# Optimization experiments

Measured on AMD Instinct MI355X. Metric: run time of the kernel, lower is better.

## Reference

```python
import jax, jax.numpy as jnp
import numpy as np
import math

TAU = math.log(2.0)   # C=2
LAM = 0.25
BATCH_SIZE = 12


def _lambertw(y, iters=20):
    """Principal-branch Lambert W for y >= -1/e via Halley iteration (on-device,
    replacing the scipy CPU roundtrip)."""
    # initial guess: series expansion near the branch point, log1p elsewhere
    w = jnp.where(
        y < 1.0,
        -1.0 + jnp.sqrt(jnp.maximum(2.0 * (jnp.e * y + 1.0), 0.0)),
        jnp.log1p(y),
    )

    def body(w, _):
        ew = jnp.exp(w)
        f = w * ew - y
        denom = ew * (w + 1.0) - (w + 2.0) * f / (2.0 * (w + 1.0) + 1e-12)
        w = jnp.where(jnp.abs(f) > 0.0, w - f / denom, w)
        return w, None

    w, _ = jax.lax.scan(body, w, None, length=iters)
    return w


def setup_inputs() -> dict:
    key = jax.random.key(0)
    n = 2097152  # rows per label group
    logits = jax.random.normal(key, (3 * n, 3), dtype=jnp.float32)
    return {"discriminator_out": logits, "n0": n, "n1": n, "n2": n}


def reference(discriminator_out, n0, n1, n2):
    # labels: n0 zeros, n1 ones, n2 twos (static sizes)
    labels = jnp.concatenate([
        jnp.zeros((n0,), jnp.int32),
        jnp.ones((n1,), jnp.int32),
        jnp.full((n2,), 2, jnp.int32),
    ])
    # per-row cross entropy (single log_softmax shared by both CE uses in the torch code)
    logp = jax.nn.log_softmax(discriminator_out, axis=-1)
    l_i = -jnp.take_along_axis(logp, labels[:, None], axis=1)[:, 0]  # [N]

    # sigma uses detached losses
    l_det = jax.lax.stop_gradient(l_i)
    y = 0.5 * jnp.maximum(-2.0 / jnp.e, (l_det - TAU) / LAM)  # y >= -1/e
    w = _lambertw(y)
    sigma = jnp.exp(-w)  # log(sigma) = -w

    loss = ((l_i - TAU) * sigma + LAM * jnp.square(w)).sum() / BATCH_SIZE
    return loss
```

## Files before the change

### kernel.cpp

```cpp
#include <hip/hip_runtime.h>
#include <math.h>

#define TBL_N     1024
#define TBL_MAXU  1023.999f
#define KIDX      44.36141955583649f
#define LOG2E     1.44269504088896340736f
#define INV_BATCH (1.0f / 12.0f)

struct TblData { float v[TBL_N + 1]; };

constexpr double k_ln2 = 0.69314718055994530942;
constexpr double k_e   = 2.71828182845904523536;

constexpr double cexp(double x) {
    double t = x * 1.44269504088896340736;
    int n = (int)(t + (t >= 0 ? 0.5 : -0.5));
    double r = x - (double)n * k_ln2;
    double s = 1.0, term = 1.0;
    for (int i = 1; i <= 13; ++i) { term *= r / i; s += term; }
    double p = 1.0;
    if (n >= 0) for (int i = 0; i <  n; ++i) p *= 2.0;
    else        for (int i = 0; i < -n; ++i) p *= 0.5;
    return s * p;
}
constexpr double csqrt_(double x) {
    double r = x > 1.0 ? x : 1.0;
    for (int i = 0; i < 24; ++i) r = 0.5 * (r + x / r);
    return r;
}
constexpr double clog_(double x) {
    int n = 0; double m = x;
    while (m >= 2.0) { m *= 0.5; ++n; }
    while (m <  1.0) { m *= 2.0; --n; }
    double z = (m - 1.0) / (m + 1.0), z2 = z * z, s = 0.0, t = z;
    for (int i = 0; i < 17; ++i) { s += t / (2 * i + 1); t *= z2; }
    return 2.0 * s + (double)n * k_ln2;
}
constexpr TblData make_table() {
    TblData T{};
    for (int i = 0; i <= TBL_N; ++i) {
        double l   = (double)i * (16.0 / TBL_N);
        double tau = k_ln2;
        double l0  = tau - 1.0 / (2.0 * k_e);
        double F;
        if (l < l0) {
            F = k_e * (l - tau) + 0.25;
        } else {
            double y = 2.0 * (l - tau);
            double ylim = -1.0 / k_e;
            if (y < ylim) y = ylim;
            double w = (y < 3.0) ? (csqrt_(2.0 * (k_e * y + 1.0)) - 1.0)
                                 : clog_(y);
            for (int it = 0; it < 4; ++it) {
                double ew  = cexp(w);
                double f   = w * ew - y;
                double wp1 = w + 1.0;
                double den = ew * wp1 - (w + 2.0) * f / (2.0 * wp1 + 1e-300);
                if (f != 0.0) w -= f / den;
            }
            F = 0.25 * ((1.0 + w) * (1.0 + w) - 1.0);
        }
        T.v[i] = (float)F;
    }
    return T;
}
__device__ __constant__ TblData c_tbl = make_table();

__shared__ float s_tbl[TBL_N + 1];

__device__ __forceinline__ float tbl_eval(float u) {
    u = fminf(u, TBL_MAXU);
    int   i = (int)u;
    float f = u - (float)i;
    float t0 = s_tbl[i];
    float t1 = s_tbl[i + 1];
    return fmaf(f, t1 - t0, t0);
}

template<int L>
__device__ __forceinline__ float row_fixed(float a, float b, float c) {
    float xl = (L == 0) ? a : ((L == 1) ? b : c);
    float o1 = (L == 0) ? b : a;
    float o2 = (L == 2) ? b : c;
    float e1 = exp2f((o1 - xl) * LOG2E);
    float e2 = exp2f((o2 - xl) * LOG2E);
    float u  = __log2f(1.0f + e1 + e2) * KIDX;
    return tbl_eval(u);
}

__device__ __forceinline__ float row_gen(float a, float b, float c, int lab) {
    float xl = (lab == 0) ? a : ((lab == 1) ? b : c);
    float o1 = (lab == 0) ? b : a;
    float o2 = (lab == 2) ? b : c;
    float e1 = exp2f((o1 - xl) * LOG2E);
    float e2 = exp2f((o2 - xl) * LOG2E);
    float u  = __log2f(1.0f + e1 + e2) * KIDX;
    return tbl_eval(u);
}

template<int L>
__device__ __forceinline__ float quad_sum(float4 f0, float4 f1, float4 f2) {
    return row_fixed<L>(f0.x, f0.y, f0.z) + row_fixed<L>(f0.w, f1.x, f1.y)
         + row_fixed<L>(f1.z, f1.w, f2.x) + row_fixed<L>(f2.y, f2.z, f2.w);
}

__device__ __forceinline__ float block_reduce(float acc) {
#pragma unroll
    for (int off = 32; off > 0; off >>= 1)
        acc += __shfl_down(acc, off, 64);
    __shared__ float sacc[4];
    int lane = threadIdx.x & 63;
    int wv   = threadIdx.x >> 6;
    if (lane == 0) sacc[wv] = acc;
    __syncthreads();
    float s = 0.0f;
    if (threadIdx.x == 0)
        s = sacc[0] + sacc[1] + sacc[2] + sacc[3];
    return s;
}

__global__ __launch_bounds__(256) void superloss_partial(
        const float* __restrict__ x,
        const int* __restrict__ pn0,
        const int* __restrict__ pn1,
        float* __restrict__ partial,
        int nrows) {
    for (int i = threadIdx.x; i <= TBL_N; i += 256)
        s_tbl[i] = c_tbl.v[i];
    __syncthreads();

    const int n0  = *pn0;
    const int n01 = n0 + *pn1;

    const int gid    = blockIdx.x * 256 + threadIdx.x;
    const int stride = gridDim.x * 256;
    const int nq     = nrows >> 2;

    float acc = 0.0f;

    if (((n0 | n01) & 3) == 0) {
        const int nq0 = n0 >> 2, nq1 = n01 >> 2;
        int q0 = gid, q1 = nq0 + gid, q2 = nq1 + gid;
        for (;;) {
            bool h0 = q0 < nq0, h1 = q1 < nq1, h2 = q2 < nq;
            if (!(h0 || h1 || h2)) break;
            float4 A0, A1, A2, B0, B1, B2, C0, C1, C2;
            if (h0) { const float4* p = (const float4*)x + 3 * (size_t)q0; A0 = p[0]; A1 = p[1]; A2 = p[2]; }
            if (h1) { const float4* p = (const float4*)x + 3 * (size_t)q1; B0 = p[0]; B1 = p[1]; B2 = p[2]; }
            if (h2) { const float4* p = (const float4*)x + 3 * (size_t)q2; C0 = p[0]; C1 = p[1]; C2 = p[2]; }
            if (h0) acc += quad_sum<0>(A0, A1, A2);
            if (h1) acc += quad_sum<1>(B0, B1, B2);
            if (h2) acc += quad_sum<2>(C0, C1, C2);
            q0 += stride; q1 += stride; q2 += stride;
        }
        for (int r = (nq << 2) + gid; r < nrows; r += stride) {
            int lab = (r >= n0) + (r >= n01);
            acc += row_gen(x[3 * (size_t)r], x[3 * (size_t)r + 1],
                           x[3 * (size_t)r + 2], lab);
        }
    } else {
        for (int r = gid; r < nrows; r += stride) {
            int lab = (r >= n0) + (r >= n01);
            acc += row_gen(x[3 * (size_t)r], x[3 * (size_t)r + 1],
                           x[3 * (size_t)r + 2], lab);
        }
    }

    float s = block_reduce(acc);
    if (threadIdx.x == 0)
        partial[blockIdx.x] = s;
}

__global__ __launch_bounds__(256) void superloss_final(
        const float* __restrict__ partial,
        int np,
        float* __restrict__ out) {
    float acc = 0.0f;
    for (int i = threadIdx.x; i < np; i += 256)
        acc += partial[i];
    float s = block_reduce(acc);
    if (threadIdx.x == 0)
        out[0] = s * INV_BATCH;
}

extern "C" void kernel_launch(void* const* d_in, const int* in_sizes, int n_in,
                              void* d_out, int out_size, void* d_ws, size_t ws_size,
                              hipStream_t stream) {
    const float* x   = (const float*)d_in[0];
    const int*   pn0 = (const int*)d_in[1];
    const int*   pn1 = (const int*)d_in[2];

    const int nrows = in_sizes[0] / 3;

    int nblk = 2048;
    size_t need = (size_t)nblk * sizeof(float);
    if (ws_size < need) {
        nblk = (int)(ws_size / sizeof(float));
        if (nblk < 1) nblk = 1;
    }

    float* partial = (float*)d_ws;
    superloss_partial<<<nblk, 256, 0, stream>>>(x, pn0, pn1, partial, nrows);
    superloss_final<<<1, 256, 0, stream>>>(partial, nblk, (float*)d_out);
}
```

Measured before the change: 109.1 us.

## Index loss table by float exponent bits, drop log and interpolation

Replaces the log2-plus-linear-interpolation lookup with a 2048-entry table indexed directly by the top mantissa and exponent bits of the softmax denominator, so each row skips the log and one of its two shared-memory reads. The 1/12 scale is folded into the table. The three interleaved label regions are now walked in separate loops instead of one combined loop. Without interpolation the piecewise-constant lookup adds approximation error, and the region loops lose the interleaving of loads across regions.

Measured after the change: 105.4 us. 3.4% less time.

```diff
diff --git a/kernel.cpp b/kernel.cpp
--- a/kernel.cpp
+++ b/kernel.cpp
@@ -1,13 +1,12 @@
 #include <hip/hip_runtime.h>
 #include <math.h>
 
-#define TBL_N     1024
-#define TBL_MAXU  1023.999f
-#define KIDX      44.36141955583649f
+#define NTB       2048
 #define LOG2E     1.44269504088896340736f
-#define INV_BATCH (1.0f / 12.0f)
-
-struct TblData { float v[TBL_N + 1]; };
+#define IDX_BIAS  0x3F80u
+#define INV_BATCH (1.0 / 12.0)
+
+struct alignas(16) TblData { float v[NTB]; };
 
 constexpr double k_ln2 = 0.69314718055994530942;
 constexpr double k_e   = 2.71828182845904523536;
@@ -25,7 +24,7 @@
 }
 constexpr double csqrt_(double x) {
     double r = x > 1.0 ? x : 1.0;
-    for (int i = 0; i < 24; ++i) r = 0.5 * (r + x / r);
+    for (int i = 0; i < 12; ++i) r = 0.5 * (r + x / r);
     return r;
 }
 constexpr double clog_(double x) {
@@ -38,70 +37,80 @@
 }
 constexpr TblData make_table() {
     TblData T{};
-    for (int i = 0; i <= TBL_N; ++i) {
-        double l   = (double)i * (16.0 / TBL_N);
-        double tau = k_ln2;
-        double l0  = tau - 1.0 / (2.0 * k_e);
+    const double tau = k_ln2;
+    const double l0  = tau - 1.0 / (2.0 * k_e);
+    double w_prev = 0.0;
+    for (int i = 0; i < NTB; ++i) {
+        int e = i >> 7, m = i & 127;
+        double s = 1.0 + ((double)m + 0.5) / 128.0;
+        for (int k = 0; k < e; ++k) s *= 2.0;
+        double l = clog_(s);
         double F;
         if (l < l0) {
             F = k_e * (l - tau) + 0.25;
         } else {
             double y = 2.0 * (l - tau);
-            double ylim = -1.0 / k_e;
-            if (y < ylim) y = ylim;
-            double w = (y < 3.0) ? (csqrt_(2.0 * (k_e * y + 1.0)) - 1.0)
-                                 : clog_(y);
-            for (int it = 0; it < 4; ++it) {
-                double ew  = cexp(w);
-                double f   = w * ew - y;
-                double wp1 = w + 1.0;
-                double den = ew * wp1 - (w + 2.0) * f / (2.0 * wp1 + 1e-300);
-                if (f != 0.0) w -= f / den;
+            double w;
+            double dy = y + 1.0 / k_e;
+            if (dy < 0.15) {
+                double p = csqrt_(2.0 * k_e * dy);
+                w = -1.0 + p - p * p / 3.0 + (11.0 / 72.0) * p * p * p;
+            } else {
+                w = w_prev;
             }
-            F = 0.25 * ((1.0 + w) * (1.0 + w) - 1.0);
+            for (int it = 0; it < 2; ++it) {
+                double ew = cexp(w);
+                w -= (w * ew - y) / (ew * (w + 1.0));
+            }
+            w_prev = w;
+            F = 0.5 * w + 0.25 * w * w;
         }
-        T.v[i] = (float)F;
+        T.v[i] = (float)(F * INV_BATCH);
     }
     return T;
 }
 __device__ __constant__ TblData c_tbl = make_table();
 
-__shared__ float s_tbl[TBL_N + 1];
-
-__device__ __forceinline__ float tbl_eval(float u) {
-    u = fminf(u, TBL_MAXU);
-    int   i = (int)u;
-    float f = u - (float)i;
-    float t0 = s_tbl[i];
-    float t1 = s_tbl[i + 1];
-    return fmaf(f, t1 - t0, t0);
-}
-
 template<int L>
-__device__ __forceinline__ float row_fixed(float a, float b, float c) {
+__device__ __forceinline__ float row_fixed(const float* __restrict__ tbl,
+                                           float a, float b, float c) {
     float xl = (L == 0) ? a : ((L == 1) ? b : c);
     float o1 = (L == 0) ? b : a;
     float o2 = (L == 2) ? b : c;
-    float e1 = exp2f((o1 - xl) * LOG2E);
-    float e2 = exp2f((o2 - xl) * LOG2E);
-    float u  = __log2f(1.0f + e1 + e2) * KIDX;
-    return tbl_eval(u);
-}
-
-__device__ __forceinline__ float row_gen(float a, float b, float c, int lab) {
+    float s  = 1.0f + exp2f((o1 - xl) * LOG2E) + exp2f((o2 - xl) * LOG2E);
+    unsigned i = (__float_as_uint(s) >> 16) - IDX_BIAS;
+    i = min(i, (unsigned)(NTB - 1));
+    return tbl[i];
+}
+
+__device__ __forceinline__ float row_gen(const float* __restrict__ tbl,
+                                         float a, float b, float c, int lab) {
     float xl = (lab == 0) ? a : ((lab == 1) ? b : c);
     float o1 = (lab == 0) ? b : a;
     float o2 = (lab == 2) ? b : c;
-    float e1 = exp2f((o1 - xl) * LOG2E);
-    float e2 = exp2f((o2 - xl) * LOG2E);
-    float u  = __log2f(1.0f + e1 + e2) * KIDX;
-    return tbl_eval(u);
+    float s  = 1.0f + exp2f((o1 - xl) * LOG2E) + exp2f((o2 - xl) * LOG2E);
+    unsigned i = (__float_as_uint(s) >> 16) - IDX_BIAS;
+    i = min(i, (unsigned)(NTB - 1));
+    return tbl[i];
 }
 
 template<int L>
-__device__ __forceinline__ float quad_sum(float4 f0, float4 f1, float4 f2) {
-    return row_fixed<L>(f0.x, f0.y, f0.z) + row_fixed<L>(f0.w, f1.x, f1.y)
-         + row_fixed<L>(f1.z, f1.w, f2.x) + row_fixed<L>(f2.y, f2.z, f2.w);
+__device__ __forceinline__ float region_sum(const float* __restrict__ x,
+                                            const float* __restrict__ tbl,
+                                            int qlo, int qhi,
+                                            int gid, int stride) {
+    float acc = 0.0f;
+    for (int q = qlo + gid; q < qhi; q += stride) {
+        const float4* p = (const float4*)x + 3 * (size_t)q;
+        float4 f0 = p[0];
+        float4 f1 = p[1];
+        float4 f2 = p[2];
+        acc += row_fixed<L>(tbl, f0.x, f0.y, f0.z);
+        acc += row_fixed<L>(tbl, f0.w, f1.x, f1.y);
+        acc += row_fixed<L>(tbl, f1.z, f1.w, f2.x);
+        acc += row_fixed<L>(tbl, f2.y, f2.z, f2.w);
+    }
+    return acc;
 }
 
 __device__ __forceinline__ float block_reduce(float acc) {
@@ -125,43 +134,38 @@
         const int* __restrict__ pn1,
         float* __restrict__ partial,
         int nrows) {
-    for (int i = threadIdx.x; i <= TBL_N; i += 256)
-        s_tbl[i] = c_tbl.v[i];
+    __shared__ float s_tbl[NTB];
+    {
+        const float4* ct = (const float4*)c_tbl.v;
+        float4* st = (float4*)s_tbl;
+        st[threadIdx.x]       = ct[threadIdx.x];
+        st[threadIdx.x + 256] = ct[threadIdx.x + 256];
+    }
     __syncthreads();
 
     const int n0  = *pn0;
     const int n01 = n0 + *pn1;
 
+    const int nq     = nrows >> 2;
     const int gid    = blockIdx.x * 256 + threadIdx.x;
     const int stride = gridDim.x * 256;
-    const int nq     = nrows >> 2;
 
     float acc = 0.0f;
 
     if (((n0 | n01) & 3) == 0) {
         const int nq0 = n0 >> 2, nq1 = n01 >> 2;
-        int q0 = gid, q1 = nq0 + gid, q2 = nq1 + gid;
-        for (;;) {
-            bool h0 = q0 < nq0, h1 = q1 < nq1, h2 = q2 < nq;
-            if (!(h0 || h1 || h2)) break;
-            float4 A0, A1, A2, B0, B1, B2, C0, C1, C2;
-            if (h0) { const float4* p = (const float4*)x + 3 * (size_t)q0; A0 = p[0]; A1 = p[1]; A2 = p[2]; }
-            if (h1) { const float4* p = (const float4*)x + 3 * (size_t)q1; B0 = p[0]; B1 = p[1]; B2 = p[2]; }
-            if (h2) { const float4* p = (const float4*)x + 3 * (size_t)q2; C0 = p[0]; C1 = p[1]; C2 = p[2]; }
-            if (h0) acc += quad_sum<0>(A0, A1, A2);
-            if (h1) acc += quad_sum<1>(B0, B1, B2);
-            if (h2) acc += quad_sum<2>(C0, C1, C2);
-            q0 += stride; q1 += stride; q2 += stride;
-        }
+        acc += region_sum<0>(x, s_tbl, 0,   nq0, gid, stride);
+        acc += region_sum<1>(x, s_tbl, nq0, nq1, gid, stride);
+        acc += region_sum<2>(x, s_tbl, nq1, nq,  gid, stride);
         for (int r = (nq << 2) + gid; r < nrows; r += stride) {
             int lab = (r >= n0) + (r >= n01);
-            acc += row_gen(x[3 * (size_t)r], x[3 * (size_t)r + 1],
+            acc += row_gen(s_tbl, x[3 * (size_t)r], x[3 * (size_t)r + 1],
                            x[3 * (size_t)r + 2], lab);
         }
     } else {
         for (int r = gid; r < nrows; r += stride) {
             int lab = (r >= n0) + (r >= n01);
-            acc += row_gen(x[3 * (size_t)r], x[3 * (size_t)r + 1],
+            acc += row_gen(s_tbl, x[3 * (size_t)r], x[3 * (size_t)r + 1],
                            x[3 * (size_t)r + 2], lab);
         }
     }
@@ -180,7 +184,7 @@
         acc += partial[i];
     float s = block_reduce(acc);
     if (threadIdx.x == 0)
-        out[0] = s * INV_BATCH;
+        out[0] = s;
 }
 
 extern "C" void kernel_launch(void* const* d_in, const int* in_sizes, int n_in,
```
